# Optimization experiments

Hardware: AMD Instinct MI355X
Metric: run time of the kernel (lower is better)

## Reference

```python
import jax, jax.numpy as jnp
import numpy as np

N = 50000   # number of cells/nodes
C = 256     # in_channels
H = 4       # num_heads
D = 64      # out_channels (per-head)
E = 800000  # number of edges (avg degree 16)


def setup_inputs() -> dict:
    key = jax.random.key(0)
    ks = jax.random.split(key, 10)
    s = 1.0 / np.sqrt(C)  # torch nn.Linear default init bound
    u = lambda k, shape: jax.random.uniform(k, shape, jnp.float32, -s, s)
    return {
        "query_input": jax.random.normal(ks[0], (N, C), jnp.float32),
        "source_input": jax.random.normal(ks[1], (N, C), jnp.float32),
        "Wq_w": u(ks[2], (H * D, C)), "Wq_b": u(ks[3], (H * D,)),
        "Wk_w": u(ks[4], (H * D, C)), "Wk_b": u(ks[5], (H * D,)),
        "Wv_w": u(ks[6], (H * D, C)), "Wv_b": u(ks[7], (H * D,)),
        "edge_index": jax.random.randint(ks[8], (2, E), 0, N),
        "edge_weight": jax.random.uniform(ks[9], (E,), jnp.float32),
    }


def reference(query_input, source_input, Wq_w, Wq_b, Wk_w, Wk_b, Wv_w, Wv_b,
              edge_index, edge_weight):
    n = query_input.shape[0]
    q = (query_input @ Wq_w.T + Wq_b).reshape(n, H, D)
    k = (source_input @ Wk_w.T + Wk_b).reshape(n, H, D)
    v = (source_input @ Wv_w.T + Wv_b).reshape(n, H, D)

    # --- linear (kernelized) attention, global Frobenius normalization ---
    qs = q / jnp.linalg.norm(q)
    ksn = k / jnp.linalg.norm(k)
    kvs = jnp.einsum('lhm,lhd->hmd', ksn, v)               # [H,M,D]
    attn_num = jnp.einsum('nhm,hmd->nhd', qs, kvs)
    attn_num = attn_num + v.sum(axis=0)[None]              # + vs_sum broadcast
    ks_sum = ksn.sum(axis=0)                               # [H,M]
    normalizer = jnp.einsum('nhm,hm->nh', qs, ks_sum)[..., None] + jnp.float32(n)
    attn_out = attn_num / normalizer                       # [N,H,D]

    # --- GCN aggregation on value: out[col] += w * d_norm_in * d_norm_out * v[row] ---
    row, col = edge_index[0], edge_index[1]
    d = jnp.zeros((n,), jnp.float32).at[col].add(1.0)      # in-degree on col
    d_norm_in = jnp.sqrt(1.0 / d[col])
    d_norm_out = jnp.sqrt(1.0 / d[row])
    val = jnp.nan_to_num(edge_weight * d_norm_in * d_norm_out,
                         nan=0.0, posinf=0.0, neginf=0.0)  # [E]
    gathered = v[row] * val[:, None, None]                 # [E,H,D]
    gcn_out = jax.ops.segment_sum(gathered, col, num_segments=n)  # [N,H,D]

    return (attn_out + gcn_out).mean(axis=1)               # [N,D]
```

## Files before the change

### kernel.cpp

```cpp
#include <hip/hip_runtime.h>
#include <hip/hip_bf16.h>

#define N_NODES 50000
#define N_EDGES 800000
#define NBUK 512
#define BWID 98
#define BCAP 2048
#define PCHUNK 4096
#define PBLK 196
#define NVS 32

typedef __bf16 bf16x8 __attribute__((ext_vector_type(8)));
typedef float f32x4 __attribute__((ext_vector_type(4)));

__device__ __forceinline__ unsigned short f2bf(float f) {
    unsigned int u = __builtin_bit_cast(unsigned int, f);
    u += 0x7fffu + ((u >> 16) & 1u);
    return (unsigned short)(u >> 16);
}
__device__ __forceinline__ float bf2f(unsigned short s) {
    return __uint_as_float((unsigned int)s << 16);
}

__device__ __forceinline__ void gld_lds16(const void* g, void* lds) {
    __builtin_amdgcn_global_load_lds(
        (const __attribute__((address_space(1))) unsigned int*)g,
        (__attribute__((address_space(3))) unsigned int*)lds, 16, 0, 0);
}

__global__ __launch_bounds__(256) void k_wprep(const float* __restrict__ Wv,
                                               const float* __restrict__ bv,
                                               unsigned short* __restrict__ wvbar,
                                               float* __restrict__ bvbar) {
    int idx = blockIdx.x * 256 + threadIdx.x;
    int d = idx >> 6;
    int c0 = (idx & 63) * 4;
    const float4* W4 = (const float4*)Wv;
    float4 w0 = W4[((d) * 256 + c0) >> 2];
    float4 w1 = W4[((64 + d) * 256 + c0) >> 2];
    float4 w2 = W4[((128 + d) * 256 + c0) >> 2];
    float4 w3 = W4[((192 + d) * 256 + c0) >> 2];
    ushort4 s;
    s.x = f2bf(0.25f * (w0.x + w1.x + w2.x + w3.x));
    s.y = f2bf(0.25f * (w0.y + w1.y + w2.y + w3.y));
    s.z = f2bf(0.25f * (w0.z + w1.z + w2.z + w3.z));
    s.w = f2bf(0.25f * (w0.w + w1.w + w2.w + w3.w));
    int ks = c0 >> 5;
    int q  = (c0 >> 3) & 3;
    int j0 = c0 & 7;
    int nf = d >> 4;
    int ln = d & 15;
    int base = ((ks * 4 + nf) * 64 + q * 16 + ln) * 8 + j0;
    *(ushort4*)&wvbar[base] = s;
    if (blockIdx.x == 0 && threadIdx.x < 64) {
        int t = threadIdx.x;
        bvbar[t] = 0.25f * (bv[t] + bv[64 + t] + bv[128 + t] + bv[192 + t]);
    }
}

__global__ __launch_bounds__(256) void k_part(const int* __restrict__ ei,
                                              const float* __restrict__ ew,
                                              int* __restrict__ gcur,
                                              uint2* __restrict__ bkt)
{
    __shared__ int hist[NBUK];
    __shared__ int s2[256];
    __shared__ int lstart[NBUK];
    __shared__ int lcur[NBUK];
    __shared__ int gbase[NBUK];
    __shared__ uint2 lent[PCHUNK];
    __shared__ unsigned int ldst[PCHUNK];
    const int t = threadIdx.x;
    const int e0 = blockIdx.x * PCHUNK;
    const int cnt = min(N_EDGES - e0, PCHUNK);

    hist[t] = 0; hist[t + 256] = 0;
    __syncthreads();
    #pragma unroll
    for (int k = 0; k < PCHUNK / 256; ++k) {
        int e = e0 + k * 256 + t;
        if (e < N_EDGES) atomicAdd(&hist[ei[N_EDGES + e] / BWID], 1);
    }
    __syncthreads();
    {
        int b = t;
        if (hist[b]) gbase[b] = b * BCAP + atomicAdd(&gcur[b], hist[b]);
        b = t + 256;
        if (hist[b]) gbase[b] = b * BCAP + atomicAdd(&gcur[b], hist[b]);
    }
    s2[t] = hist[2 * t] + hist[2 * t + 1];
    __syncthreads();
    #pragma unroll
    for (int d = 1; d < 256; d <<= 1) {
        int u = (t >= d) ? s2[t - d] : 0;
        __syncthreads();
        s2[t] += u;
        __syncthreads();
    }
    {
        int b0 = (t > 0) ? s2[t - 1] : 0;
        lstart[2 * t] = b0;
        lstart[2 * t + 1] = b0 + hist[2 * t];
        lcur[2 * t] = b0;
        lcur[2 * t + 1] = b0 + hist[2 * t];
    }
    __syncthreads();
    #pragma unroll
    for (int k = 0; k < PCHUNK / 256; ++k) {
        int e = e0 + k * 256 + t;
        if (e < N_EDGES) {
            int c = ei[N_EDGES + e];
            int b = c / BWID;
            int lp = atomicAdd(&lcur[b], 1);
            uint2 en;
            en.x = ((unsigned int)ei[e] << 16) | (unsigned int)f2bf(ew[e]);
            en.y = (unsigned int)(c - b * BWID);
            lent[lp] = en;
            unsigned int gd = (unsigned int)(gbase[b] + (lp - lstart[b]));
            ldst[lp] = (gd < (unsigned int)((b + 1) * BCAP)) ? gd : 0xFFFFFFFFu;
        }
    }
    __syncthreads();
    for (int j = t; j < cnt; j += 256) {
        unsigned int gd = ldst[j];
        if (gd != 0xFFFFFFFFu) bkt[gd] = lent[j];
    }
}

__global__ __launch_bounds__(256) void k_bucket(const int* __restrict__ gcur,
                                                const uint2* __restrict__ bkt,
                                                int* __restrict__ deg,
                                                int* __restrict__ off,
                                                unsigned int* __restrict__ srt)
{
    __shared__ int hist[128];
    __shared__ int lcur[128];
    __shared__ unsigned int stg[BCAP];
    const int t = threadIdx.x;
    const int b = blockIdx.x;
    if (t < 128) hist[t] = 0;
    __syncthreads();
    const int cnt = min(gcur[b], BCAP);
    const uint2* base = bkt + (size_t)b * BCAP;
    for (int i = t; i < cnt; i += 256)
        atomicAdd(&hist[base[i].y], 1);
    __syncthreads();
    const int v = (t < 128) ? hist[t] : 0;
    #pragma unroll
    for (int d = 1; d < 128; d <<= 1) {
        int u = (t >= d && t < 128) ? hist[t - d] : 0;
        __syncthreads();
        if (t >= d && t < 128) hist[t] += u;
        __syncthreads();
    }
    if (t < 128) {
        int excl = hist[t] - v;
        lcur[t] = excl;
        if (t < BWID) {
            int col = b * BWID + t;
            if (col < N_NODES) {
                deg[col] = v;
                off[col] = b * BCAP + excl;
            }
        }
    }
    __syncthreads();
    for (int i = t; i < cnt; i += 256) {
        uint2 en = base[i];
        int pos = atomicAdd(&lcur[en.y], 1);
        stg[pos] = en.x;
    }
    __syncthreads();
    unsigned int* sb = srt + (size_t)b * BCAP;
    for (int i = t; i < cnt; i += 256) sb[i] = stg[i];
}

__global__ __launch_bounds__(256) void k_vbar(
    const float* __restrict__ Xs, const unsigned short* __restrict__ wvbar,
    const float* __restrict__ bvbar, const int* __restrict__ deg,
    unsigned short* __restrict__ vbarh, float* __restrict__ vsumr)
{
    __shared__ float lX[64 * 128];
    const int t = threadIdx.x;
    const int w = t >> 6;
    const int l = t & 63;
    const int ln = l & 15;
    const int q = l >> 4;
    const int n0 = blockIdx.x * 64;

    const char* Xc = (const char*)Xs;
    const bf16x8* Wf = (const bf16x8*)wvbar;
    const unsigned int swzl = ((unsigned int)(ln & 7)) << 4;
    const char* lrow = (const char*)&lX[(w * 16 + ln) * 128];

    f32x4 acc[4];
    #pragma unroll
    for (int nf = 0; nf < 4; ++nf) acc[nf] = (f32x4){0.f, 0.f, 0.f, 0.f};

    #pragma unroll
    for (int h = 0; h < 2; ++h) {
        #pragma unroll
        for (int i = 0; i < 8; ++i) {
            int r = w * 16 + i * 2 + (l >> 5);
            int g = n0 + r;
            int gc = (g < N_NODES) ? g : 0;
            unsigned int off = ((unsigned int)((l & 31) * 16))
                             ^ (((unsigned int)(r & 7)) << 4);
            const void* src = Xc + (size_t)gc * 1024 + (unsigned int)(h * 512) + off;
            gld_lds16(src, &lX[(w * 16 + i * 2) * 128]);
        }
        asm volatile("s_waitcnt vmcnt(0)" ::: "memory");
        __builtin_amdgcn_sched_barrier(0);

        #pragma unroll
        for (int ks2 = 0; ks2 < 4; ++ks2) {
            unsigned int c0 = (unsigned int)(ks2 * 128 + q * 32);
            float4 xa = *(const float4*)(lrow + (c0 ^ swzl));
            float4 xb = *(const float4*)(lrow + ((c0 + 16u) ^ swzl));
            bf16x8 A;
            A[0] = (__bf16)xa.x; A[1] = (__bf16)xa.y;
            A[2] = (__bf16)xa.z; A[3] = (__bf16)xa.w;
            A[4] = (__bf16)xb.x; A[5] = (__bf16)xb.y;
            A[6] = (__bf16)xb.z; A[7] = (__bf16)xb.w;
            int ks = h * 4 + ks2;
            #pragma unroll
            for (int nf = 0; nf < 4; ++nf) {
                bf16x8 b = Wf[(ks * 4 + nf) * 64 + l];
                acc[nf] = __builtin_amdgcn_mfma_f32_16x16x32_bf16(A, b, acc[nf], 0, 0, 0);
            }
        }
        if (h == 0) {
            asm volatile("s_waitcnt lgkmcnt(0)" ::: "memory");
            __builtin_amdgcn_sched_barrier(0);
        }
    }

    float bvb[4];
    #pragma unroll
    for (int nf = 0; nf < 4; ++nf) bvb[nf] = bvbar[nf * 16 + ln];
    float psum[4] = {0.f, 0.f, 0.f, 0.f};
    #pragma unroll
    for (int r4 = 0; r4 < 4; ++r4) {
        int g = n0 + w * 16 + q * 4 + r4;
        bool ok = g < N_NODES;
        float sc = 0.f;
        if (ok) {
            float dg = (float)deg[g];
            sc = (dg > 0.f) ? __frsqrt_rn(dg) : 0.f;
        }
        #pragma unroll
        for (int nf = 0; nf < 4; ++nf) {
            if (ok) {
                vbarh[g * 64 + nf * 16 + ln] = f2bf((acc[nf][r4] + bvb[nf]) * sc);
                psum[nf] += acc[nf][r4];
            }
        }
    }
    #pragma unroll
    for (int nf = 0; nf < 4; ++nf) {
        float v = psum[nf];
        v += __shfl_xor(v, 16, 64);
        v += __shfl_xor(v, 32, 64);
        psum[nf] = v;
    }
    if (l < 16) {
        int rep = (blockIdx.x * 4 + w) & (NVS - 1);
        #pragma unroll
        for (int nf = 0; nf < 4; ++nf)
            atomicAdd(&vsumr[rep * 64 + nf * 16 + ln], psum[nf]);
    }
}

__global__ __launch_bounds__(256) void k_gather(
    const int* __restrict__ off, const int* __restrict__ deg,
    const unsigned int* __restrict__ srt, const unsigned short* __restrict__ vbarh,
    const float* __restrict__ vsumr, const float* __restrict__ bvbar,
    float* __restrict__ out)
{
    const int t = threadIdx.x;
    const int lane = t & 63;
    const int n = blockIdx.x * 4 + (t >> 6);
    if (n >= N_NODES) return;
    const int e0 = off[n];
    const int dc = deg[n];
    const int e1 = e0 + dc;
    float acc = 0.f;
    int e = e0;
    for (; e + 3 < e1; e += 4) {
        unsigned int p0 = srt[e];
        unsigned int p1 = srt[e + 1];
        unsigned int p2 = srt[e + 2];
        unsigned int p3 = srt[e + 3];
        float a0 = __uint_as_float(p0 << 16) * bf2f(vbarh[(p0 >> 16) * 64 + lane]);
        float a1 = __uint_as_float(p1 << 16) * bf2f(vbarh[(p1 >> 16) * 64 + lane]);
        float a2 = __uint_as_float(p2 << 16) * bf2f(vbarh[(p2 >> 16) * 64 + lane]);
        float a3 = __uint_as_float(p3 << 16) * bf2f(vbarh[(p3 >> 16) * 64 + lane]);
        acc += (a0 + a1) + (a2 + a3);
    }
    for (; e < e1; ++e) {
        unsigned int p = srt[e];
        acc += __uint_as_float(p << 16) * bf2f(vbarh[(p >> 16) * 64 + lane]);
    }
    float dcf = (float)dc;
    float scn = (dcf > 0.f) ? __frsqrt_rn(dcf) : 0.f;
    float vs = 0.f;
    #pragma unroll
    for (int i = 0; i < NVS; ++i) vs += vsumr[i * 64 + lane];
    float aconst = vs * (1.0f / (float)N_NODES) + bvbar[lane];
    out[n * 64 + lane] = acc * scn + aconst;
}

extern "C" void kernel_launch(void* const* d_in, const int* in_sizes, int n_in,
                              void* d_out, int out_size, void* d_ws, size_t ws_size,
                              hipStream_t stream)
{
    const float* Xs = (const float*)d_in[1];
    const float* Wv = (const float*)d_in[6];
    const float* bv = (const float*)d_in[7];
    const int*   ei = (const int*)d_in[8];
    const float* ew = (const float*)d_in[9];
    float* out = (float*)d_out;

    unsigned short* vbarh = (unsigned short*)d_ws;
    uint2* bkt  = (uint2*)(vbarh + (size_t)N_NODES * 64);
    unsigned int* srt = (unsigned int*)(bkt + (size_t)NBUK * BCAP);
    unsigned short* wvbar = (unsigned short*)(srt + (size_t)NBUK * BCAP);
    float* bvbar   = (float*)(wvbar + 16384);
    float* vsumr   = bvbar + 64;
    int*   gcur    = (int*)(vsumr + NVS * 64);
    int*   deg     = gcur + NBUK;
    int*   off     = deg + N_NODES;

    hipMemsetAsync(vsumr, 0, (size_t)(NVS * 64 + NBUK) * 4, stream);
    k_wprep<<<16, 256, 0, stream>>>(Wv, bv, wvbar, bvbar);
    k_part<<<PBLK, 256, 0, stream>>>(ei, ew, gcur, bkt);
    k_bucket<<<NBUK, 256, 0, stream>>>(gcur, bkt, deg, off, srt);
    k_vbar<<<(N_NODES + 63) / 64, 256, 0, stream>>>(Xs, wvbar, bvbar, deg, vbarh, vsumr);
    k_gather<<<(NBUK * BWID) / 4, 256, 0, stream>>>(off, deg, srt, vbarh, vsumr, bvbar, out);
}
```

Baseline: 210.5 us.

## Fold memset into prep kernel, cache edge data in LDS, halve partition chunk

Removes the separate hipMemsetAsync by zeroing gcur and vsumr inside k_wprep. k_part now caches column indices in LDS so they are not re-read from global memory, and uses smaller chunks across more blocks. k_bucket stages bucket entries in LDS instead of reading them twice, and k_gather unrolls the edge loop to 8 for more memory-level parallelism. Extra LDS use may lower occupancy, and the smaller chunks add more global atomics on gcur.

```diff
diff --git a/kernel.cpp b/kernel.cpp
--- a/kernel.cpp
+++ b/kernel.cpp
@@ -6,8 +6,8 @@
 #define NBUK 512
 #define BWID 98
 #define BCAP 2048
-#define PCHUNK 4096
-#define PBLK 196
+#define PCHUNK 2048
+#define PBLK 391
 #define NVS 32
 
 typedef __bf16 bf16x8 __attribute__((ext_vector_type(8)));
@@ -31,7 +31,9 @@
 __global__ __launch_bounds__(256) void k_wprep(const float* __restrict__ Wv,
                                                const float* __restrict__ bv,
                                                unsigned short* __restrict__ wvbar,
-                                               float* __restrict__ bvbar) {
+                                               float* __restrict__ bvbar,
+                                               int* __restrict__ gcur,
+                                               float* __restrict__ vsumr) {
     int idx = blockIdx.x * 256 + threadIdx.x;
     int d = idx >> 6;
     int c0 = (idx & 63) * 4;
@@ -56,6 +58,12 @@
         int t = threadIdx.x;
         bvbar[t] = 0.25f * (bv[t] + bv[64 + t] + bv[128 + t] + bv[192 + t]);
     }
+    if (blockIdx.x == 1) {
+        for (int i = threadIdx.x; i < NBUK; i += 256) gcur[i] = 0;
+    }
+    if (blockIdx.x == 2) {
+        for (int i = threadIdx.x; i < NVS * 64; i += 256) vsumr[i] = 0.f;
+    }
 }
 
 __global__ __launch_bounds__(256) void k_part(const int* __restrict__ ei,
@@ -68,6 +76,7 @@
     __shared__ int lstart[NBUK];
     __shared__ int lcur[NBUK];
     __shared__ int gbase[NBUK];
+    __shared__ unsigned short scol[PCHUNK];
     __shared__ uint2 lent[PCHUNK];
     __shared__ unsigned int ldst[PCHUNK];
     const int t = threadIdx.x;
@@ -78,8 +87,13 @@
     __syncthreads();
     #pragma unroll
     for (int k = 0; k < PCHUNK / 256; ++k) {
-        int e = e0 + k * 256 + t;
-        if (e < N_EDGES) atomicAdd(&hist[ei[N_EDGES + e] / BWID], 1);
+        int idx = k * 256 + t;
+        int e = e0 + idx;
+        if (e < N_EDGES) {
+            int c = ei[N_EDGES + e];
+            scol[idx] = (unsigned short)c;
+            atomicAdd(&hist[c / BWID], 1);
+        }
     }
     __syncthreads();
     {
@@ -107,9 +121,10 @@
     __syncthreads();
     #pragma unroll
     for (int k = 0; k < PCHUNK / 256; ++k) {
-        int e = e0 + k * 256 + t;
+        int idx = k * 256 + t;
+        int e = e0 + idx;
         if (e < N_EDGES) {
-            int c = ei[N_EDGES + e];
+            int c = (int)scol[idx];
             int b = c / BWID;
             int lp = atomicAdd(&lcur[b], 1);
             uint2 en;
@@ -135,6 +150,7 @@
 {
     __shared__ int hist[128];
     __shared__ int lcur[128];
+    __shared__ uint2 ent[BCAP];
     __shared__ unsigned int stg[BCAP];
     const int t = threadIdx.x;
     const int b = blockIdx.x;
@@ -142,8 +158,11 @@
     __syncthreads();
     const int cnt = min(gcur[b], BCAP);
     const uint2* base = bkt + (size_t)b * BCAP;
-    for (int i = t; i < cnt; i += 256)
-        atomicAdd(&hist[base[i].y], 1);
+    for (int i = t; i < cnt; i += 256) {
+        uint2 en = base[i];
+        ent[i] = en;
+        atomicAdd(&hist[en.y], 1);
+    }
     __syncthreads();
     const int v = (t < 128) ? hist[t] : 0;
     #pragma unroll
@@ -166,7 +185,7 @@
     }
     __syncthreads();
     for (int i = t; i < cnt; i += 256) {
-        uint2 en = base[i];
+        uint2 en = ent[i];
         int pos = atomicAdd(&lcur[en.y], 1);
         stg[pos] = en.x;
     }
@@ -286,16 +305,24 @@
     const int e1 = e0 + dc;
     float acc = 0.f;
     int e = e0;
-    for (; e + 3 < e1; e += 4) {
+    for (; e + 7 < e1; e += 8) {
         unsigned int p0 = srt[e];
         unsigned int p1 = srt[e + 1];
         unsigned int p2 = srt[e + 2];
         unsigned int p3 = srt[e + 3];
+        unsigned int p4 = srt[e + 4];
+        unsigned int p5 = srt[e + 5];
+        unsigned int p6 = srt[e + 6];
+        unsigned int p7 = srt[e + 7];
         float a0 = __uint_as_float(p0 << 16) * bf2f(vbarh[(p0 >> 16) * 64 + lane]);
         float a1 = __uint_as_float(p1 << 16) * bf2f(vbarh[(p1 >> 16) * 64 + lane]);
         float a2 = __uint_as_float(p2 << 16) * bf2f(vbarh[(p2 >> 16) * 64 + lane]);
         float a3 = __uint_as_float(p3 << 16) * bf2f(vbarh[(p3 >> 16) * 64 + lane]);
-        acc += (a0 + a1) + (a2 + a3);
+        float a4 = __uint_as_float(p4 << 16) * bf2f(vbarh[(p4 >> 16) * 64 + lane]);
+        float a5 = __uint_as_float(p5 << 16) * bf2f(vbarh[(p5 >> 16) * 64 + lane]);
+        float a6 = __uint_as_float(p6 << 16) * bf2f(vbarh[(p6 >> 16) * 64 + lane]);
+        float a7 = __uint_as_float(p7 << 16) * bf2f(vbarh[(p7 >> 16) * 64 + lane]);
+        acc += ((a0 + a1) + (a2 + a3)) + ((a4 + a5) + (a6 + a7));
     }
     for (; e < e1; ++e) {
         unsigned int p = srt[e];
@@ -331,8 +358,7 @@
     int*   deg     = gcur + NBUK;
     int*   off     = deg + N_NODES;
 
-    hipMemsetAsync(vsumr, 0, (size_t)(NVS * 64 + NBUK) * 4, stream);
-    k_wprep<<<16, 256, 0, stream>>>(Wv, bv, wvbar, bvbar);
+    k_wprep<<<16, 256, 0, stream>>>(Wv, bv, wvbar, bvbar, gcur, vsumr);
     k_part<<<PBLK, 256, 0, stream>>>(ei, ew, gcur, bkt);
     k_bucket<<<NBUK, 256, 0, stream>>>(gcur, bkt, deg, off, srt);
     k_vbar<<<(N_NODES + 63) / 64, 256, 0, stream>>>(Xs, wvbar, bvbar, deg, vbarh, vsumr);
```

After: 197.9 us. -6.0%, faster.
